# Kernel tuning notes

Hardware: AMD Instinct MI355X
Metric: run time of the kernel (lower is better)

## Reference

```python
import jax, jax.numpy as jnp
import numpy as np

# Supernet configuration (matches init_kwargs)
HIDDEN = [1024, 2048]
HEADS = [8, 16]
ABITS = [4, 8]
WBITS = [4, 8]
B, S = 4, 4096
MAX_IN = max(HIDDEN)            # 2048
MAX_OUT = max(HIDDEN)           # min(heads)*max(hidden)//min(heads) = 2048


def fake_quant(v, s, bit):
    """LSQ-style symmetric fake quantization with straight-through rounding."""
    qp = float(2 ** (bit - 1) - 1)
    qn = -float(2 ** (bit - 1))
    vs = jnp.clip(v / s, qn, qp)
    vq = vs + jax.lax.stop_gradient(jnp.round(vs) - vs)  # STE round
    return vq * s


def setup_inputs() -> dict:
    key = jax.random.key(0)
    k1, k2, k3, k4 = jax.random.split(key, 4)
    x = jax.random.normal(k1, (B, S, MAX_IN), jnp.float32)
    weights = jax.random.uniform(k2, (16,), jnp.float32)  # arch mixing coeffs
    W = jax.random.normal(k3, (MAX_OUT, MAX_IN), jnp.float32) * 0.02
    b = jax.random.normal(k4, (MAX_OUT,), jnp.float32) * 0.02
    # init_weight_scale: LSQ init 2*mean(|W|)/sqrt(Qp) per weight bitwidth
    w_scales = jnp.stack([2.0 * jnp.mean(jnp.abs(W)) / jnp.sqrt(float(2 ** (bit - 1) - 1))
                          for bit in WBITS])
    a_scales = jnp.ones((len(ABITS),), jnp.float32)
    return {"x": x, "weights": weights, "W": W, "b": b,
            "a_scales": a_scales, "w_scales": w_scales}


def reference(x, weights, W, b, a_scales, w_scales):
    # Non-argmax mixture path (reverse=False):
    # for each (hidden_i, heads_j, abit_m, wbit_n): slice W to
    # [out_dim, in_dim], zero-pad to [MAX_OUT, MAX_IN] (== masking, since
    # per-tensor fake-quant maps 0 -> 0), quantize, and weighted-accumulate.
    # Quantized x / W depend only on abit / wbit, so compute each once.
    qx = [fake_quant(x, a_scales[m], ABITS[m]) for m in range(len(ABITS))]   # [B,S,MAX_IN]
    qw = [fake_quant(W, w_scales[n], WBITS[n]) for n in range(len(WBITS))]  # [MAX_OUT,MAX_IN]
    out_idx = jnp.arange(MAX_OUT)
    in_idx = jnp.arange(MAX_IN)

    w_mix = jnp.zeros_like(W)
    x_mix = jnp.zeros_like(x)
    b_mix = jnp.zeros_like(b)
    k = 0
    for i, h in enumerate(HIDDEN):
        for j, nh in enumerate(HEADS):
            head_dim = h // nh
            out_dim = nh * head_dim  # == h when divisible
            in_dim = h
            wmask = (out_idx[:, None] < out_dim) & (in_idx[None, :] < in_dim)
            bmask = out_idx < out_dim
            for m in range(len(ABITS)):
                for n in range(len(WBITS)):
                    a = weights[k]
                    w_mix = w_mix + a * jnp.where(wmask, qw[n], 0.0)
                    x_mix = x_mix + a * qx[m]
                    b_mix = b_mix + a * jnp.where(bmask, b, 0.0)
                    k += 1
    # out = F.linear(x_mix, w_mix, b_mix)
    out = jnp.einsum('bsi,oi->bso', x_mix, w_mix) + b_mix
    return out
```

## Files before the change

### kernel.cpp

```cpp
#include <hip/hip_runtime.h>
#include <hip/hip_bf16.h>
#include <stdint.h>

#define MDIM 16384
#define NDIM 2048
#define KDIM 2048

typedef __attribute__((ext_vector_type(4))) float f32x4;
typedef __attribute__((ext_vector_type(8))) short s16x8;

__device__ __forceinline__ void gload_lds16(const __hip_bfloat16* g, void* l) {
    __builtin_amdgcn_global_load_lds(
        (const __attribute__((address_space(1))) void*)g,
        (__attribute__((address_space(3))) void*)l,
        16, 0, 0);
}


__global__ __launch_bounds__(256) void prep_x(
    const float* __restrict__ x, const float* __restrict__ weights,
    const float* __restrict__ a_scales, __hip_bfloat16* __restrict__ xq)
{
    float A0 = 0.f, A1 = 0.f;
    #pragma unroll
    for (int k = 0; k < 16; ++k) {
        float w = weights[k];
        if (((k >> 1) & 1) == 0) A0 += w; else A1 += w;
    }
    const float s0 = a_scales[0], s1 = a_scales[1];
    const float r0 = 1.f / s0, r1 = 1.f / s1;

    size_t idx = ((size_t)blockIdx.x * 256 + threadIdx.x) * 8;
    const f32x4* xv = (const f32x4*)(x + idx);
    f32x4 v0 = xv[0], v1 = xv[1];
    float vals[8] = {v0.x, v0.y, v0.z, v0.w, v1.x, v1.y, v1.z, v1.w};

    union { s16x8 v; __hip_bfloat16 h[8]; } u;
    #pragma unroll
    for (int j = 0; j < 8; ++j) {
        float q0 = rintf(fminf(fmaxf(vals[j] * r0, -8.f),   7.f)) * s0;
        float q1 = rintf(fminf(fmaxf(vals[j] * r1, -128.f), 127.f)) * s1;
        u.h[j] = __float2bfloat16(A0 * q0 + A1 * q1);
    }
    *(s16x8*)(xq + idx) = u.v;
}

__global__ __launch_bounds__(256) void prep_w(
    const float* __restrict__ W, const float* __restrict__ weights,
    const float* __restrict__ w_scales, __hip_bfloat16* __restrict__ wq)
{
    float c00 = weights[0] + weights[2]  + weights[4]  + weights[6];
    float c01 = weights[1] + weights[3]  + weights[5]  + weights[7];
    float c10 = weights[8] + weights[10] + weights[12] + weights[14];
    float c11 = weights[9] + weights[11] + weights[13] + weights[15];

    const float s0 = w_scales[0], s1 = w_scales[1];
    const float r0 = 1.f / s0, r1 = 1.f / s1;

    size_t idx = ((size_t)blockIdx.x * 256 + threadIdx.x) * 8;
    const int o = (int)(idx >> 11);
    const int c = (int)(idx & 2047);
    const bool inner = (o < 1024) && (c < 1024);
    const float k0 = inner ? (c00 + c10) : c10;
    const float k1 = inner ? (c01 + c11) : c11;

    const f32x4* wv = (const f32x4*)(W + idx);
    f32x4 v0 = wv[0], v1 = wv[1];
    float vals[8] = {v0.x, v0.y, v0.z, v0.w, v1.x, v1.y, v1.z, v1.w};

    union { s16x8 v; __hip_bfloat16 h[8]; } u;
    #pragma unroll
    for (int j = 0; j < 8; ++j) {
        float q0 = rintf(fminf(fmaxf(vals[j] * r0, -8.f),   7.f)) * s0;
        float q1 = rintf(fminf(fmaxf(vals[j] * r1, -128.f), 127.f)) * s1;
        u.h[j] = __float2bfloat16(k0 * q0 + k1 * q1);
    }
    *(s16x8*)(wq + idx) = u.v;
}

__global__ __launch_bounds__(256) void prep_b(
    const float* __restrict__ b, const float* __restrict__ weights,
    float* __restrict__ bm)
{
    int o = blockIdx.x * 256 + threadIdx.x;
    if (o >= NDIM) return;
    float S1 = 0.f, S0 = 0.f;
    #pragma unroll
    for (int k = 0; k < 8; ++k)  S0 += weights[k];
    #pragma unroll
    for (int k = 8; k < 16; ++k) S1 += weights[k];
    bm[o] = b[o] * ((o < 1024) ? (S0 + S1) : S1);
}


#define BM 256
#define BN 256
#define NCH 64
#define ASLOT 16384
#define BREG  65536

#define MFMA(a, b, c) __builtin_amdgcn_mfma_f32_16x16x32_bf16((a), (b), (c), 0, 0, 0)

#define CHUNK(S, T)                                                          \
  {                                                                          \
    asm volatile("" ::: "memory");      \
    s16x8 af[8], bf[4];                                                      \
    _Pragma("unroll")                                                        \
    for (int m_ = 0; m_ < 8; ++m_)                                           \
      af[m_] = *(const s16x8*)(lds + (S) * ASLOT + aoff + m_ * 1024);        \
    _Pragma("unroll")                                                        \
    for (int n_ = 0; n_ < 4; ++n_)                                           \
      bf[n_] = *(const s16x8*)(lds + BREG + (S) * ASLOT + boff + n_ * 1024); \
    gload_lds16(As0 + kg * 32, lds + (T) * ASLOT + ldoff);                   \
    gload_lds16(As1 + kg * 32, lds + (T) * ASLOT + 8192 + ldoff);            \
    gload_lds16(Bs0 + kg * 32, lds + BREG + (T) * ASLOT + ldoff);            \
    gload_lds16(Bs1 + kg * 32, lds + BREG + (T) * ASLOT + 8192 + ldoff);     \
    kg = (kg + 1) & (NCH - 1);                                               \
    __builtin_amdgcn_s_setprio(1);                                           \
    _Pragma("unroll")                                                        \
    for (int m_ = 0; m_ < 8; ++m_) {                                         \
      acc[m_][0] = MFMA(af[m_], bf[0], acc[m_][0]);                          \
      acc[m_][1] = MFMA(af[m_], bf[1], acc[m_][1]);                          \
      acc[m_][2] = MFMA(af[m_], bf[2], acc[m_][2]);                          \
      acc[m_][3] = MFMA(af[m_], bf[3], acc[m_][3]);                          \
    }                                                                        \
    __builtin_amdgcn_s_setprio(0);                                           \
    asm volatile("s_waitcnt vmcnt(8)" ::: "memory");   \
    __builtin_amdgcn_s_barrier();                                            \
  }

__global__ __launch_bounds__(512, 2) void gemm256(
    const __hip_bfloat16* __restrict__ A,
    const __hip_bfloat16* __restrict__ B,
    const float* __restrict__ bias,
    float* __restrict__ C)
{
    __shared__ char lds[8 * ASLOT];

    const int tid  = threadIdx.x;
    const int lane = tid & 63;
    const int wid  = tid >> 6;
    const int wm   = wid >> 2;
    const int wn   = wid & 3;

    const int bid  = blockIdx.x;
    const int swz  = (bid & 7) * 64 + (bid >> 3);
    const int brow = (swz >> 3) * BM;
    const int bcol = (swz & 7) * BN;

    const int csw = (tid & 3) ^ ((tid >> 3) & 3);
    const __hip_bfloat16* As0 = A + (size_t)(brow + (tid >> 2)) * KDIM + csw * 8;
    const __hip_bfloat16* As1 = As0 + (size_t)128 * KDIM;
    const __hip_bfloat16* Bs0 = B + (size_t)(bcol + (tid >> 2)) * KDIM + csw * 8;
    const __hip_bfloat16* Bs1 = Bs0 + (size_t)128 * KDIM;
    const int ldoff = tid * 16;

    const int fr  = lane & 15;
    const int l16 = lane >> 4;
    const int xr  = (l16 ^ ((fr >> 1) & 3)) * 16;
    const int aoff = (wm * 128 + fr) * 64 + xr;
    const int boff = (wn * 64  + fr) * 64 + xr;

    f32x4 acc[8][4];
    #pragma unroll
    for (int m = 0; m < 8; ++m)
        #pragma unroll
        for (int n = 0; n < 4; ++n)
            acc[m][n] = (f32x4){0.f, 0.f, 0.f, 0.f};

    int kg = 3;

    #pragma unroll
    for (int q = 0; q < 3; ++q) {
        gload_lds16(As0 + q * 32, lds + q * ASLOT + ldoff);
        gload_lds16(As1 + q * 32, lds + q * ASLOT + 8192 + ldoff);
        gload_lds16(Bs0 + q * 32, lds + BREG + q * ASLOT + ldoff);
        gload_lds16(Bs1 + q * 32, lds + BREG + q * ASLOT + 8192 + ldoff);
    }
    asm volatile("s_waitcnt vmcnt(8)" ::: "memory");
    __builtin_amdgcn_s_barrier();

    #pragma unroll 1
    for (int it = 0; it < NCH / 4; ++it) {
        CHUNK(0, 3);
        CHUNK(1, 0);
        CHUNK(2, 1);
        CHUNK(3, 2);
    }
    asm volatile("s_waitcnt vmcnt(0) lgkmcnt(0)" ::: "memory");

    const int ccol0 = bcol + wn * 64 + fr;
    const int crow0 = brow + wm * 128 + l16 * 4;
    float bv[4];
    #pragma unroll
    for (int n = 0; n < 4; ++n) bv[n] = bias[ccol0 + n * 16];

    #pragma unroll
    for (int m = 0; m < 8; ++m) {
        #pragma unroll
        for (int j = 0; j < 4; ++j) {
            float* Crow = C + (size_t)(crow0 + m * 16 + j) * NDIM;
            #pragma unroll
            for (int n = 0; n < 4; ++n)
                Crow[ccol0 + n * 16] = acc[m][n][j] + bv[n];
        }
    }
}


extern "C" void kernel_launch(void* const* d_in, const int* in_sizes, int n_in,
                              void* d_out, int out_size, void* d_ws, size_t ws_size,
                              hipStream_t stream) {
    const float* x        = (const float*)d_in[0];
    const float* weights  = (const float*)d_in[1];
    const float* W        = (const float*)d_in[2];
    const float* b        = (const float*)d_in[3];
    const float* a_scales = (const float*)d_in[4];
    const float* w_scales = (const float*)d_in[5];
    float* out = (float*)d_out;

    __hip_bfloat16* xq = (__hip_bfloat16*)d_ws;
    __hip_bfloat16* wq = (__hip_bfloat16*)((char*)d_ws + 67108864);
    float*          bm = (float*)((char*)d_ws + 67108864 + 8388608);

    prep_w<<<dim3((NDIM * KDIM) / (256 * 8)), dim3(256), 0, stream>>>(W, weights, w_scales, wq);
    prep_b<<<dim3(NDIM / 256), dim3(256), 0, stream>>>(b, weights, bm);
    prep_x<<<dim3(((size_t)MDIM * KDIM) / (256 * 8)), dim3(256), 0, stream>>>(x, weights, a_scales, xq);
    gemm256<<<dim3((MDIM / BM) * (NDIM / BN)), dim3(512), 0, stream>>>(xq, wq, bm, out);
}
```

Before: 162.5 us.

## Software-pipeline LDS fragment loads across MFMA phases with register double buffering

Each K-chunk is split into four phases. Each phase issues MFMAs on the current A/B fragments while loading the next phase's A fragments, and the next chunk's B fragments, from LDS into ping-pong registers. Global-to-LDS loads are spread one per phase instead of bunched together, and the first fragments are preloaded before the loop. Because the next chunk's LDS slot is now read early, the wait is tightened to vmcnt(4), which reduces the number of global loads allowed in flight. The intent is to hide LDS read latency behind matrix instructions, at the cost of more complex register scheduling and less slack on global loads.

```diff
diff --git a/kernel.cpp b/kernel.cpp
--- a/kernel.cpp
+++ b/kernel.cpp
@@ -101,32 +101,45 @@
 
 #define MFMA(a, b, c) __builtin_amdgcn_mfma_f32_16x16x32_bf16((a), (b), (c), 0, 0, 0)
 
-#define CHUNK(S, T)                                                          \
+#define FENCE asm volatile("" ::: "memory")
+
+#define PHASE(P, S, S1, T, AFU, AFL, BFU, BFL)                               \
   {                                                                          \
-    asm volatile("" ::: "memory");      \
-    s16x8 af[8], bf[4];                                                      \
-    _Pragma("unroll")                                                        \
-    for (int m_ = 0; m_ < 8; ++m_)                                           \
-      af[m_] = *(const s16x8*)(lds + (S) * ASLOT + aoff + m_ * 1024);        \
-    _Pragma("unroll")                                                        \
-    for (int n_ = 0; n_ < 4; ++n_)                                           \
-      bf[n_] = *(const s16x8*)(lds + BREG + (S) * ASLOT + boff + n_ * 1024); \
-    gload_lds16(As0 + kg * 32, lds + (T) * ASLOT + ldoff);                   \
-    gload_lds16(As1 + kg * 32, lds + (T) * ASLOT + 8192 + ldoff);            \
-    gload_lds16(Bs0 + kg * 32, lds + BREG + (T) * ASLOT + ldoff);            \
-    gload_lds16(Bs1 + kg * 32, lds + BREG + (T) * ASLOT + 8192 + ldoff);     \
+    if ((P) < 3) {                                                           \
+      AFL[0] = *(const s16x8*)(lds + (S) * ASLOT + aoff + (2*(P)+2) * 1024); \
+      AFL[1] = *(const s16x8*)(lds + (S) * ASLOT + aoff + (2*(P)+3) * 1024); \
+    } else {                                                                 \
+      AFL[0] = *(const s16x8*)(lds + (S1) * ASLOT + aoff);                   \
+      AFL[1] = *(const s16x8*)(lds + (S1) * ASLOT + aoff + 1024);            \
+    }                                                                        \
+    BFL[P] = *(const s16x8*)(lds + BREG + (S1) * ASLOT + boff + (P) * 1024); \
+    if ((P) == 0) gload_lds16(As0 + kg * 32, lds + (T) * ASLOT + ldoff);     \
+    if ((P) == 1) gload_lds16(As1 + kg * 32, lds + (T) * ASLOT + 8192 + ldoff); \
+    if ((P) == 2) gload_lds16(Bs0 + kg * 32, lds + BREG + (T) * ASLOT + ldoff); \
+    if ((P) == 3) gload_lds16(Bs1 + kg * 32, lds + BREG + (T) * ASLOT + 8192 + ldoff); \
+    FENCE;                                                                   \
+    __builtin_amdgcn_s_setprio(1);                                           \
+    acc[2*(P)][0]   = MFMA(AFU[0], BFU[0], acc[2*(P)][0]);                   \
+    acc[2*(P)][1]   = MFMA(AFU[0], BFU[1], acc[2*(P)][1]);                   \
+    acc[2*(P)][2]   = MFMA(AFU[0], BFU[2], acc[2*(P)][2]);                   \
+    acc[2*(P)][3]   = MFMA(AFU[0], BFU[3], acc[2*(P)][3]);                   \
+    acc[2*(P)+1][0] = MFMA(AFU[1], BFU[0], acc[2*(P)+1][0]);                 \
+    acc[2*(P)+1][1] = MFMA(AFU[1], BFU[1], acc[2*(P)+1][1]);                 \
+    acc[2*(P)+1][2] = MFMA(AFU[1], BFU[2], acc[2*(P)+1][2]);                 \
+    acc[2*(P)+1][3] = MFMA(AFU[1], BFU[3], acc[2*(P)+1][3]);                 \
+    __builtin_amdgcn_s_setprio(0);                                           \
+  }
+
+#define CHUNK(S, S1, T, BFU, BFL)                                            \
+  {                                                                          \
+    PHASE(0, S, S1, T, afP0, afP1, BFU, BFL);                                \
+    PHASE(1, S, S1, T, afP1, afP0, BFU, BFL);                                \
+    PHASE(2, S, S1, T, afP0, afP1, BFU, BFL);                                \
+    PHASE(3, S, S1, T, afP1, afP0, BFU, BFL);                                \
     kg = (kg + 1) & (NCH - 1);                                               \
-    __builtin_amdgcn_s_setprio(1);                                           \
-    _Pragma("unroll")                                                        \
-    for (int m_ = 0; m_ < 8; ++m_) {                                         \
-      acc[m_][0] = MFMA(af[m_], bf[0], acc[m_][0]);                          \
-      acc[m_][1] = MFMA(af[m_], bf[1], acc[m_][1]);                          \
-      acc[m_][2] = MFMA(af[m_], bf[2], acc[m_][2]);                          \
-      acc[m_][3] = MFMA(af[m_], bf[3], acc[m_][3]);                          \
-    }                                                                        \
-    __builtin_amdgcn_s_setprio(0);                                           \
-    asm volatile("s_waitcnt vmcnt(8)" ::: "memory");   \
+    asm volatile("s_waitcnt vmcnt(4)" ::: "memory");                         \
     __builtin_amdgcn_s_barrier();                                            \
+    FENCE;                                                                   \
   }
 
 __global__ __launch_bounds__(512, 2) void gemm256(
@@ -168,6 +181,7 @@
         for (int n = 0; n < 4; ++n)
             acc[m][n] = (f32x4){0.f, 0.f, 0.f, 0.f};
 
+    s16x8 afP0[2], afP1[2], bfA[4], bfB[4];
     int kg = 3;
 
     #pragma unroll
@@ -177,15 +191,21 @@
         gload_lds16(Bs0 + q * 32, lds + BREG + q * ASLOT + ldoff);
         gload_lds16(Bs1 + q * 32, lds + BREG + q * ASLOT + 8192 + ldoff);
     }
-    asm volatile("s_waitcnt vmcnt(8)" ::: "memory");
+    asm volatile("s_waitcnt vmcnt(4)" ::: "memory");
     __builtin_amdgcn_s_barrier();
+    FENCE;
+    afP0[0] = *(const s16x8*)(lds + aoff);
+    afP0[1] = *(const s16x8*)(lds + aoff + 1024);
+    #pragma unroll
+    for (int n = 0; n < 4; ++n)
+        bfA[n] = *(const s16x8*)(lds + BREG + boff + n * 1024);
 
     #pragma unroll 1
     for (int it = 0; it < NCH / 4; ++it) {
-        CHUNK(0, 3);
-        CHUNK(1, 0);
-        CHUNK(2, 1);
-        CHUNK(3, 2);
+        CHUNK(0, 1, 3, bfA, bfB);
+        CHUNK(1, 2, 0, bfB, bfA);
+        CHUNK(2, 3, 1, bfA, bfB);
+        CHUNK(3, 0, 2, bfB, bfA);
     }
     asm volatile("s_waitcnt vmcnt(0) lgkmcnt(0)" ::: "memory");
 
```

Measured after the change: 161.5 us. About the same (-0.6%).

## Load A fragments directly from global into registers, staging only B in LDS

Applied to the files above, without the earlier changes.

Each wave now reads its A operand fragments straight from global memory into registers, one K-step ahead, and stages only the B tile through LDS. This halves LDS usage and removes the A LDS write/read traffic. B fragments are double-buffered in registers so the MFMAs overlap the next loads. In exchange the A reads are strided, uncoalesced 16-byte global loads per lane, register pressure rises from double-buffering both operands, and the vmcnt accounting now mixes A register loads with B LDS loads.

```diff
diff --git a/kernel.cpp b/kernel.cpp
--- a/kernel.cpp
+++ b/kernel.cpp
@@ -96,36 +96,33 @@
 #define BM 256
 #define BN 256
 #define NCH 64
-#define ASLOT 16384
-#define BREG  65536
+#define BSLOT 16384
 
 #define MFMA(a, b, c) __builtin_amdgcn_mfma_f32_16x16x32_bf16((a), (b), (c), 0, 0, 0)
 
-#define CHUNK(S, T)                                                          \
+#define CHUNK(AFU, AFL, BFU, BFL, SB1, SB3)                                  \
   {                                                                          \
-    asm volatile("" ::: "memory");      \
-    s16x8 af[8], bf[4];                                                      \
+    const size_t au_ = (size_t)kgA * 64;                                     \
     _Pragma("unroll")                                                        \
     for (int m_ = 0; m_ < 8; ++m_)                                           \
-      af[m_] = *(const s16x8*)(lds + (S) * ASLOT + aoff + m_ * 1024);        \
+      AFL[m_] = *(const s16x8*)(Abase + au_ + (size_t)m_ * 65536);           \
+    gload_lds16(Bs0 + kgB * 32, lds + (SB3) * BSLOT + ldoff);                \
+    gload_lds16(Bs1 + kgB * 32, lds + (SB3) * BSLOT + 8192 + ldoff);         \
     _Pragma("unroll")                                                        \
     for (int n_ = 0; n_ < 4; ++n_)                                           \
-      bf[n_] = *(const s16x8*)(lds + BREG + (S) * ASLOT + boff + n_ * 1024); \
-    gload_lds16(As0 + kg * 32, lds + (T) * ASLOT + ldoff);                   \
-    gload_lds16(As1 + kg * 32, lds + (T) * ASLOT + 8192 + ldoff);            \
-    gload_lds16(Bs0 + kg * 32, lds + BREG + (T) * ASLOT + ldoff);            \
-    gload_lds16(Bs1 + kg * 32, lds + BREG + (T) * ASLOT + 8192 + ldoff);     \
-    kg = (kg + 1) & (NCH - 1);                                               \
+      BFL[n_] = *(const s16x8*)(lds + (SB1) * BSLOT + boff + n_ * 1024);     \
+    kgA = (kgA + 1) & (NCH - 1);                                             \
+    kgB = (kgB + 1) & (NCH - 1);                                             \
     __builtin_amdgcn_s_setprio(1);                                           \
     _Pragma("unroll")                                                        \
     for (int m_ = 0; m_ < 8; ++m_) {                                         \
-      acc[m_][0] = MFMA(af[m_], bf[0], acc[m_][0]);                          \
-      acc[m_][1] = MFMA(af[m_], bf[1], acc[m_][1]);                          \
-      acc[m_][2] = MFMA(af[m_], bf[2], acc[m_][2]);                          \
-      acc[m_][3] = MFMA(af[m_], bf[3], acc[m_][3]);                          \
+      acc[m_][0] = MFMA(AFU[m_], BFU[0], acc[m_][0]);                        \
+      acc[m_][1] = MFMA(AFU[m_], BFU[1], acc[m_][1]);                        \
+      acc[m_][2] = MFMA(AFU[m_], BFU[2], acc[m_][2]);                        \
+      acc[m_][3] = MFMA(AFU[m_], BFU[3], acc[m_][3]);                        \
     }                                                                        \
     __builtin_amdgcn_s_setprio(0);                                           \
-    asm volatile("s_waitcnt vmcnt(8)" ::: "memory");   \
+    asm volatile("s_waitcnt vmcnt(10)" ::: "memory");                        \
     __builtin_amdgcn_s_barrier();                                            \
   }
 
@@ -135,7 +132,7 @@
     const float* __restrict__ bias,
     float* __restrict__ C)
 {
-    __shared__ char lds[8 * ASLOT];
+    __shared__ char lds[4 * BSLOT];
 
     const int tid  = threadIdx.x;
     const int lane = tid & 63;
@@ -149,8 +146,6 @@
     const int bcol = (swz & 7) * BN;
 
     const int csw = (tid & 3) ^ ((tid >> 3) & 3);
-    const __hip_bfloat16* As0 = A + (size_t)(brow + (tid >> 2)) * KDIM + csw * 8;
-    const __hip_bfloat16* As1 = As0 + (size_t)128 * KDIM;
     const __hip_bfloat16* Bs0 = B + (size_t)(bcol + (tid >> 2)) * KDIM + csw * 8;
     const __hip_bfloat16* Bs1 = Bs0 + (size_t)128 * KDIM;
     const int ldoff = tid * 16;
@@ -158,8 +153,9 @@
     const int fr  = lane & 15;
     const int l16 = lane >> 4;
     const int xr  = (l16 ^ ((fr >> 1) & 3)) * 16;
-    const int aoff = (wm * 128 + fr) * 64 + xr;
-    const int boff = (wn * 64  + fr) * 64 + xr;
+    const int boff = (wn * 64 + fr) * 64 + xr;
+    const char* Abase = (const char*)(A
+        + (size_t)(brow + wm * 128 + fr) * KDIM + l16 * 8);
 
     f32x4 acc[8][4];
     #pragma unroll
@@ -168,24 +164,30 @@
         for (int n = 0; n < 4; ++n)
             acc[m][n] = (f32x4){0.f, 0.f, 0.f, 0.f};
 
-    int kg = 3;
-
+    s16x8 afA[8], afB[8], bfA[4], bfB[4];
+    int kgA, kgB;
+
+    #pragma unroll
+    for (int m = 0; m < 8; ++m)
+        afA[m] = *(const s16x8*)(Abase + (size_t)m * 65536);
     #pragma unroll
     for (int q = 0; q < 3; ++q) {
-        gload_lds16(As0 + q * 32, lds + q * ASLOT + ldoff);
-        gload_lds16(As1 + q * 32, lds + q * ASLOT + 8192 + ldoff);
-        gload_lds16(Bs0 + q * 32, lds + BREG + q * ASLOT + ldoff);
-        gload_lds16(Bs1 + q * 32, lds + BREG + q * ASLOT + 8192 + ldoff);
-    }
-    asm volatile("s_waitcnt vmcnt(8)" ::: "memory");
+        gload_lds16(Bs0 + q * 32, lds + q * BSLOT + ldoff);
+        gload_lds16(Bs1 + q * 32, lds + q * BSLOT + 8192 + ldoff);
+    }
+    kgA = 1; kgB = 3;
+    asm volatile("s_waitcnt vmcnt(0)" ::: "memory");
     __builtin_amdgcn_s_barrier();
+    #pragma unroll
+    for (int n = 0; n < 4; ++n)
+        bfA[n] = *(const s16x8*)(lds + boff + n * 1024);
 
     #pragma unroll 1
     for (int it = 0; it < NCH / 4; ++it) {
-        CHUNK(0, 3);
-        CHUNK(1, 0);
-        CHUNK(2, 1);
-        CHUNK(3, 2);
+        CHUNK(afA, afB, bfA, bfB, 1, 3);
+        CHUNK(afB, afA, bfB, bfA, 2, 0);
+        CHUNK(afA, afB, bfA, bfB, 3, 1);
+        CHUNK(afB, afA, bfB, bfA, 0, 2);
     }
     asm volatile("s_waitcnt vmcnt(0) lgkmcnt(0)" ::: "memory");
 
```

Result: slower. 346.3 us (+113.1%).

## Shrink GEMM tile to 128x256 with 4 waves and triple-buffered LDS

Applied to the files above, without the earlier changes.

Replaces the 256x256 tile GEMM (8 waves, 4-stage LDS ring) with a 128x256 tile run by 4 waves, each computing a 128x64 slice, and a 3-stage LDS ring. The grid doubles to 1024 blocks, which improves load balance over the CUs and lowers LDS per block. In exchange, each B element is reused across fewer rows and the prefetch depth drops from 3 chunks to 2, so the kernel may become more memory-bound or expose more load latency.

```diff
diff --git a/kernel.cpp b/kernel.cpp
--- a/kernel.cpp
+++ b/kernel.cpp
@@ -93,11 +93,10 @@
 }
 
 
-#define BM 256
-#define BN 256
 #define NCH 64
-#define ASLOT 16384
-#define BREG  65536
+#define ASLOT 8192
+#define BSLOT 16384
+#define BREG  24576
 
 #define MFMA(a, b, c) __builtin_amdgcn_mfma_f32_16x16x32_bf16((a), (b), (c), 0, 0, 0)
 
@@ -110,11 +109,13 @@
       af[m_] = *(const s16x8*)(lds + (S) * ASLOT + aoff + m_ * 1024);        \
     _Pragma("unroll")                                                        \
     for (int n_ = 0; n_ < 4; ++n_)                                           \
-      bf[n_] = *(const s16x8*)(lds + BREG + (S) * ASLOT + boff + n_ * 1024); \
-    gload_lds16(As0 + kg * 32, lds + (T) * ASLOT + ldoff);                   \
-    gload_lds16(As1 + kg * 32, lds + (T) * ASLOT + 8192 + ldoff);            \
-    gload_lds16(Bs0 + kg * 32, lds + BREG + (T) * ASLOT + ldoff);            \
-    gload_lds16(Bs1 + kg * 32, lds + BREG + (T) * ASLOT + 8192 + ldoff);     \
+      bf[n_] = *(const s16x8*)(lds + BREG + (S) * BSLOT + boff + n_ * 1024); \
+    gload_lds16(As + kg * 32,                lds + (T) * ASLOT + ldoff);     \
+    gload_lds16(As + 64 * KDIM + kg * 32,    lds + (T) * ASLOT + 4096 + ldoff); \
+    _Pragma("unroll")                                                        \
+    for (int q_ = 0; q_ < 4; ++q_)                                           \
+      gload_lds16(Bs + q_ * 64 * KDIM + kg * 32,                             \
+                  lds + BREG + (T) * BSLOT + q_ * 4096 + ldoff);             \
     kg = (kg + 1) & (NCH - 1);                                               \
     __builtin_amdgcn_s_setprio(1);                                           \
     _Pragma("unroll")                                                        \
@@ -125,41 +126,37 @@
       acc[m_][3] = MFMA(af[m_], bf[3], acc[m_][3]);                          \
     }                                                                        \
     __builtin_amdgcn_s_setprio(0);                                           \
-    asm volatile("s_waitcnt vmcnt(8)" ::: "memory");   \
+    asm volatile("s_waitcnt vmcnt(6)" ::: "memory");         \
     __builtin_amdgcn_s_barrier();                                            \
   }
 
-__global__ __launch_bounds__(512, 2) void gemm256(
+__global__ __launch_bounds__(256, 2) void gemm128x256(
     const __hip_bfloat16* __restrict__ A,
     const __hip_bfloat16* __restrict__ B,
     const float* __restrict__ bias,
     float* __restrict__ C)
 {
-    __shared__ char lds[8 * ASLOT];
+    __shared__ char lds[3 * ASLOT + 3 * BSLOT];
 
     const int tid  = threadIdx.x;
     const int lane = tid & 63;
-    const int wid  = tid >> 6;
-    const int wm   = wid >> 2;
-    const int wn   = wid & 3;
+    const int wn   = tid >> 6;
 
     const int bid  = blockIdx.x;
-    const int swz  = (bid & 7) * 64 + (bid >> 3);
-    const int brow = (swz >> 3) * BM;
-    const int bcol = (swz & 7) * BN;
+    const int swz  = (bid & 7) * 128 + (bid >> 3);
+    const int brow = (swz >> 3) * 128;
+    const int bcol = (swz & 7) * 256;
 
     const int csw = (tid & 3) ^ ((tid >> 3) & 3);
-    const __hip_bfloat16* As0 = A + (size_t)(brow + (tid >> 2)) * KDIM + csw * 8;
-    const __hip_bfloat16* As1 = As0 + (size_t)128 * KDIM;
-    const __hip_bfloat16* Bs0 = B + (size_t)(bcol + (tid >> 2)) * KDIM + csw * 8;
-    const __hip_bfloat16* Bs1 = Bs0 + (size_t)128 * KDIM;
+    const __hip_bfloat16* As = A + (size_t)(brow + (tid >> 2)) * KDIM + csw * 8;
+    const __hip_bfloat16* Bs = B + (size_t)(bcol + (tid >> 2)) * KDIM + csw * 8;
     const int ldoff = tid * 16;
 
     const int fr  = lane & 15;
     const int l16 = lane >> 4;
     const int xr  = (l16 ^ ((fr >> 1) & 3)) * 16;
-    const int aoff = (wm * 128 + fr) * 64 + xr;
-    const int boff = (wn * 64  + fr) * 64 + xr;
+    const int aoff = fr * 64 + xr;
+    const int boff = (wn * 64 + fr) * 64 + xr;
 
     f32x4 acc[8][4];
     #pragma unroll
@@ -168,29 +165,32 @@
         for (int n = 0; n < 4; ++n)
             acc[m][n] = (f32x4){0.f, 0.f, 0.f, 0.f};
 
-    int kg = 3;
-
-    #pragma unroll
-    for (int q = 0; q < 3; ++q) {
-        gload_lds16(As0 + q * 32, lds + q * ASLOT + ldoff);
-        gload_lds16(As1 + q * 32, lds + q * ASLOT + 8192 + ldoff);
-        gload_lds16(Bs0 + q * 32, lds + BREG + q * ASLOT + ldoff);
-        gload_lds16(Bs1 + q * 32, lds + BREG + q * ASLOT + 8192 + ldoff);
-    }
-    asm volatile("s_waitcnt vmcnt(8)" ::: "memory");
+    int kg;
+
+    #pragma unroll
+    for (int q = 0; q < 2; ++q) {
+        gload_lds16(As + q * 32,             lds + q * ASLOT + ldoff);
+        gload_lds16(As + 64 * KDIM + q * 32, lds + q * ASLOT + 4096 + ldoff);
+        #pragma unroll
+        for (int p = 0; p < 4; ++p)
+            gload_lds16(Bs + p * 64 * KDIM + q * 32,
+                        lds + BREG + q * BSLOT + p * 4096 + ldoff);
+    }
+    kg = 2;
+    asm volatile("s_waitcnt vmcnt(6)" ::: "memory");
     __builtin_amdgcn_s_barrier();
 
     #pragma unroll 1
-    for (int it = 0; it < NCH / 4; ++it) {
-        CHUNK(0, 3);
+    for (int it = 0; it < 21; ++it) {
+        CHUNK(0, 2);
         CHUNK(1, 0);
         CHUNK(2, 1);
-        CHUNK(3, 2);
-    }
+    }
+    CHUNK(0, 2);
     asm volatile("s_waitcnt vmcnt(0) lgkmcnt(0)" ::: "memory");
 
     const int ccol0 = bcol + wn * 64 + fr;
-    const int crow0 = brow + wm * 128 + l16 * 4;
+    const int crow0 = brow + l16 * 4;
     float bv[4];
     #pragma unroll
     for (int n = 0; n < 4; ++n) bv[n] = bias[ccol0 + n * 16];
@@ -226,5 +226,5 @@
     prep_w<<<dim3((NDIM * KDIM) / (256 * 8)), dim3(256), 0, stream>>>(W, weights, w_scales, wq);
     prep_b<<<dim3(NDIM / 256), dim3(256), 0, stream>>>(b, weights, bm);
     prep_x<<<dim3(((size_t)MDIM * KDIM) / (256 * 8)), dim3(256), 0, stream>>>(x, weights, a_scales, xq);
-    gemm256<<<dim3((MDIM / BM) * (NDIM / BN)), dim3(512), 0, stream>>>(xq, wq, bm, out);
-}
+    gemm128x256<<<dim3((MDIM / 128) * (NDIM / 256)), dim3(256), 0, stream>>>(xq, wq, bm, out);
+}
```

After: 174.3 us. +7.3%, slower.
